# Kernel tuning notes

Hardware: AMD Instinct MI355X
Metric: run time of the kernel (lower is better)

Reference implementation:

```python
import jax, jax.numpy as jnp
import numpy as np

B, E, DM = 2, 1024, 512          # batch, n_edges, d_model
H, DK, DV = 8, 64, 64            # heads, d_k, d_v
MAX_NEIGHBOR = 5                 # == attn_max_dist
LN_EPS = 1e-6
NEG = -1e9


def setup_inputs() -> dict:
    key = jax.random.key(0)
    ks = jax.random.split(key, 9)
    s = 0.02
    return {
        "x": jax.random.normal(ks[0], (B, DM, E, 1), jnp.float32),
        "dist": jax.random.randint(ks[1], (B, E, E), 0, 12, jnp.int32),
        "base_rpr": jax.random.normal(ks[2], (MAX_NEIGHBOR + 1, DK), jnp.float32) * s,
        "w_q": jax.random.normal(ks[3], (DM, H * DK), jnp.float32) * s,
        "w_k": jax.random.normal(ks[4], (DM, H * DK), jnp.float32) * s,
        "w_v": jax.random.normal(ks[5], (DM, H * DV), jnp.float32) * s,
        "w_fc": jax.random.normal(ks[6], (H * DV, DM), jnp.float32) * s,
        "ln_g": jnp.ones((DM,), jnp.float32),
        "ln_b": jnp.zeros((DM,), jnp.float32),
    }


def reference(x, dist, base_rpr, w_q, w_k, w_v, w_fc, ln_g, ln_b):
    temp = jnp.asarray(DK, x.dtype) ** 0.5
    # local-attention mask (dist <= attn_max_dist); all edges valid (same-size meshes)
    mask = dist <= MAX_NEIGHBOR                      # [B,E,E] bool

    s = jnp.transpose(x[..., 0], (0, 2, 1))          # [B,E,DM]
    residual = s

    # LayerNorm applied to q only (as in the torch module)
    mu = s.mean(-1, keepdims=True)
    var = ((s - mu) ** 2).mean(-1, keepdims=True)
    qn = (s - mu) / jnp.sqrt(var + LN_EPS) * ln_g + ln_b

    q = (qn @ w_q).reshape(B, E, H, DK).transpose(0, 2, 1, 3)   # [B,H,E,DK]
    k = (s @ w_k).reshape(B, E, H, DK).transpose(0, 2, 1, 3)
    v = (s @ w_v).reshape(B, E, H, DV).transpose(0, 2, 1, 3)

    # relative-position representations gathered by (clipped) distance
    rpr = base_rpr[jnp.minimum(dist, MAX_NEIGHBOR)]  # [B,E,E,DK]

    qs = q / temp
    attn1 = jnp.einsum("bhid,bhjd->bhij", qs, k)
    attn2 = jnp.einsum("bhid,bijd->bhij", qs, rpr)
    logits = jnp.where(mask[:, None], attn1 + attn2, NEG)
    attn = jax.nn.softmax(logits, axis=-1)           # [B,H,E,E]

    out = jnp.einsum("bhij,bhjd->bhid", attn, v)     # [B,H,E,DV]
    out = out.transpose(0, 2, 1, 3).reshape(B, E, H * DV) @ w_fc + residual
    x_out = out.transpose(0, 2, 1)[..., None]        # [B,DM,E,1]

    mf = mask[:, None].astype(attn.dtype)            # [B,1,E,E]
    attn_per_edge = (attn * mf).sum((1, 2)) / mf.sum((1, 2))  # [B,E]
    return x_out, attn, attn_per_edge
```

## Files before the change

kernel.cpp:

```cpp
#include <hip/hip_runtime.h>

#define NB_B 2
#define NB_E 1024
#define NB_DM 512
#define NB_H 8
#define NEGV -1e9f

typedef __attribute__((ext_vector_type(8))) __bf16 bf16x8;
typedef __attribute__((ext_vector_type(8))) unsigned short u16x8;
typedef __attribute__((ext_vector_type(4))) float f32x4;

static __device__ __forceinline__ float bf2f(unsigned short u){
  union { unsigned int i; float f; } v; v.i = ((unsigned int)u) << 16; return v.f;
}
static __device__ __forceinline__ unsigned short f2bf(float f){
  union { float f; unsigned int i; } v; v.f = f;
  unsigned int r = v.i + 0x7FFFu + ((v.i >> 16) & 1u);
  return (unsigned short)(r >> 16);
}
static __device__ __forceinline__ f32x4 mfma16(bf16x8 a, bf16x8 b, f32x4 c){
  return __builtin_amdgcn_mfma_f32_16x16x32_bf16(a, b, c, 0, 0, 0);
}

__global__ void k_transpose_x(const float* __restrict__ x, unsigned short* __restrict__ s_bf){
  __shared__ float tile[32][33];
  const int b = blockIdx.z;
  const int d0 = blockIdx.y * 32;
  const int e0 = blockIdx.x * 32;
  const int tx = threadIdx.x, ty = threadIdx.y;
  #pragma unroll
  for (int r = 0; r < 4; ++r){
    const int d = d0 + ty + r*8;
    tile[ty + r*8][tx] = x[((size_t)b*NB_DM + d)*NB_E + e0 + tx];
  }
  __syncthreads();
  #pragma unroll
  for (int r = 0; r < 4; ++r){
    const int e = e0 + ty + r*8;
    s_bf[((size_t)b*NB_E + e)*NB_DM + d0 + tx] = f2bf(tile[tx][ty + r*8]);
  }
}

__global__ void k_transpose_w(const float* __restrict__ w0, const float* __restrict__ w1,
                              const float* __restrict__ w2, const float* __restrict__ w3,
                              unsigned short* __restrict__ wT){
  __shared__ float tile[32][33];
  const int which = blockIdx.z;
  const float* w = which==0 ? w0 : which==1 ? w1 : which==2 ? w2 : w3;
  unsigned short* dst = wT + (size_t)which*512*512;
  const int k0 = blockIdx.y*32, n0 = blockIdx.x*32;
  const int tx = threadIdx.x, ty = threadIdx.y;
  #pragma unroll
  for (int r = 0; r < 4; ++r)
    tile[ty + r*8][tx] = w[(size_t)(k0 + ty + r*8)*512 + n0 + tx];
  __syncthreads();
  #pragma unroll
  for (int r = 0; r < 4; ++r)
    dst[(size_t)(n0 + ty + r*8)*512 + k0 + tx] = f2bf(tile[tx][ty + r*8]);
}

__global__ __launch_bounds__(64) void k_ln(const unsigned short* __restrict__ s_bf,
    unsigned short* __restrict__ qn_bf, const float* __restrict__ gg, const float* __restrict__ bb){
  const int row = blockIdx.x, l = threadIdx.x;
  const unsigned short* sp = s_bf + (size_t)row*512 + l*8;
  u16x8 v = *(const u16x8*)sp;
  float f[8]; float sum = 0.f, sq = 0.f;
  #pragma unroll
  for (int i = 0; i < 8; ++i){ f[i] = bf2f(v[i]); sum += f[i]; sq += f[i]*f[i]; }
  #pragma unroll
  for (int off = 32; off >= 1; off >>= 1){
    sum += __shfl_xor(sum, off);
    sq  += __shfl_xor(sq, off);
  }
  const float mu  = sum * (1.f/512.f);
  const float var = sq * (1.f/512.f) - mu*mu;
  const float rstd = rsqrtf(var + 1e-6f);
  const float4 g0 = *(const float4*)(gg + l*8);
  const float4 g1 = *(const float4*)(gg + l*8 + 4);
  const float4 b0 = *(const float4*)(bb + l*8);
  const float4 b1 = *(const float4*)(bb + l*8 + 4);
  const float gv[8] = {g0.x,g0.y,g0.z,g0.w,g1.x,g1.y,g1.z,g1.w};
  const float bv[8] = {b0.x,b0.y,b0.z,b0.w,b1.x,b1.y,b1.z,b1.w};
  u16x8 o;
  #pragma unroll
  for (int i = 0; i < 8; ++i) o[i] = f2bf((f[i]-mu)*rstd*gv[i] + bv[i]);
  *(u16x8*)(qn_bf + (size_t)row*512 + l*8) = o;
}

__global__ void k_dist8(const int* __restrict__ dist, unsigned char* __restrict__ d8){
  const int idx = blockIdx.x*256 + threadIdx.x;
  const int4 d = ((const int4*)dist)[idx];
  uchar4 o;
  o.x = (unsigned char)(d.x <= 5 ? d.x : 6);
  o.y = (unsigned char)(d.y <= 5 ? d.y : 6);
  o.z = (unsigned char)(d.z <= 5 ? d.z : 6);
  o.w = (unsigned char)(d.w <= 5 ? d.w : 6);
  ((uchar4*)d8)[idx] = o;
}

__global__ void k_cnt(const unsigned char* __restrict__ d8, int* __restrict__ cnt){
  const int b = blockIdx.y;
  const int i0 = blockIdx.x*32;
  const int tid = threadIdx.x;
  #pragma unroll
  for (int jj = 0; jj < 4; ++jj){
    const int j = tid + jj*256;
    int c = 0;
    #pragma unroll 8
    for (int i = 0; i < 32; ++i)
      c += (d8[((size_t)b*NB_E + i0 + i)*NB_E + j] < 6) ? 1 : 0;
    atomicAdd(&cnt[b*NB_E + j], c);
  }
}

__global__ __launch_bounds__(256) void k_qr(const unsigned short* __restrict__ Q,
    const float* __restrict__ base_rpr, float* __restrict__ qr){
  __shared__ float rl[384];
  const int tid = threadIdx.x;
  for (int t = tid; t < 384; t += 256) rl[t] = base_rpr[t];
  __syncthreads();
  const int g = blockIdx.x*256 + tid;
  const unsigned short* qp = Q + (size_t)g*64;
  float qv[64];
  #pragma unroll
  for (int i = 0; i < 8; ++i){
    u16x8 v = *(const u16x8*)(qp + i*8);
    #pragma unroll
    for (int j = 0; j < 8; ++j) qv[i*8+j] = bf2f(v[j]);
  }
  #pragma unroll
  for (int c = 0; c < 6; ++c){
    float sacc = 0.f;
    #pragma unroll
    for (int d = 0; d < 64; ++d) sacc += qv[d]*rl[c*64 + d];
    qr[(size_t)g*8 + c] = sacc;
  }
}

template<int MODE>
__global__ __launch_bounds__(256) void k_gemm(
    const unsigned short* __restrict__ A, const unsigned short* __restrict__ BT,
    unsigned short* __restrict__ dst_bf, float* __restrict__ dst_f,
    const float* __restrict__ resid)
{
  const int tid = threadIdx.x;
  const int l = tid & 63, wv = tid >> 6;
  const int ll = l & 15, lg = l >> 4;
  const int m0 = blockIdx.x*64 + wv*16;
  const int n0 = blockIdx.y*64;
  const unsigned short* arow = A + (size_t)(m0 + ll)*512 + lg*8;
  f32x4 acc[4];
  #pragma unroll
  for (int nt = 0; nt < 4; ++nt) acc[nt] = (f32x4){0.f,0.f,0.f,0.f};
  #pragma unroll
  for (int ks = 0; ks < 16; ++ks){
    bf16x8 a = *(const bf16x8*)(arow + ks*32);
    #pragma unroll
    for (int nt = 0; nt < 4; ++nt){
      bf16x8 bv = *(const bf16x8*)(BT + (size_t)(n0 + nt*16 + ll)*512 + ks*32 + lg*8);
      acc[nt] = mfma16(a, bv, acc[nt]);
    }
  }
  const int rbase = m0 + lg*4;
  const int bidx = rbase >> 10;
  const int e = rbase & 1023;
  #pragma unroll
  for (int nt = 0; nt < 4; ++nt){
    const int n = n0 + nt*16 + ll;
    if (MODE == 0 || MODE == 1){
      const int h = n >> 6, dk = n & 63;
      unsigned short* dp = dst_bf + (((size_t)bidx*NB_H + h)*NB_E + e)*64 + dk;
      #pragma unroll
      for (int r = 0; r < 4; ++r)
        dp[(size_t)r*64] = f2bf(MODE == 0 ? acc[nt][r]*0.125f : acc[nt][r]);
    } else if (MODE == 2){
      const int h = n >> 6, dv = n & 63;
      ushort4 ov;
      ov.x = f2bf(acc[nt][0]); ov.y = f2bf(acc[nt][1]);
      ov.z = f2bf(acc[nt][2]); ov.w = f2bf(acc[nt][3]);
      *(ushort4*)(dst_bf + (((size_t)bidx*NB_H + h)*64 + dv)*NB_E + e) = ov;
    } else {
      const float* xr = resid + ((size_t)bidx*NB_DM + n)*NB_E + e;
      const float4 rv = *(const float4*)xr;
      const float4 ov = make_float4(acc[nt][0]+rv.x, acc[nt][1]+rv.y,
                                    acc[nt][2]+rv.z, acc[nt][3]+rv.w);
      *(float4*)(dst_f + ((size_t)bidx*NB_DM + n)*NB_E + e) = ov;
    }
  }
}

__global__ __launch_bounds__(256, 2) void k_attn(
    const unsigned short* __restrict__ Q, const unsigned short* __restrict__ K,
    const unsigned short* __restrict__ VT, const float* __restrict__ qr,
    const unsigned char* __restrict__ d8, float* __restrict__ attn_out,
    unsigned short* __restrict__ outb, float* __restrict__ ape_acc)
{
  __shared__ __align__(16) unsigned char smem[65536];
  unsigned short* plds = (unsigned short*)smem;
  float* qr_l = (float*)smem;
  float* redm = (float*)(smem + 768);
  float* reds = (float*)(smem + 1280);

  const int tid = threadIdx.x;
  const int l = tid & 63, w = tid >> 6;
  const int lg = l >> 4, ll = l & 15;
  const int bh = blockIdx.y;
  const int b = bh >> 3;
  const int ib = blockIdx.x << 5;

  for (int t = tid; t < 32*6; t += 256)
    qr_l[t] = qr[((size_t)bh*NB_E + ib + (t/6))*8 + (t % 6)];

  const unsigned short* Qb = Q + ((size_t)bh*NB_E + ib)*64;
  bf16x8 qf[2][2];
  #pragma unroll
  for (int it = 0; it < 2; ++it)
    #pragma unroll
    for (int hf = 0; hf < 2; ++hf)
      qf[it][hf] = *(const bf16x8*)(Qb + (size_t)(it*16 + ll)*64 + hf*32 + lg*8);
  __syncthreads();

  f32x4 s[2][16];
  const unsigned short* Kb = K + (size_t)bh*NB_E*64;
  #pragma unroll
  for (int jt = 0; jt < 16; ++jt){
    const int jrow = (w*16 + jt)*16 + ll;
    bf16x8 k0 = *(const bf16x8*)(Kb + (size_t)jrow*64 + lg*8);
    bf16x8 k1 = *(const bf16x8*)(Kb + (size_t)jrow*64 + 32 + lg*8);
    #pragma unroll
    for (int it = 0; it < 2; ++it){
      f32x4 acc = {0.f,0.f,0.f,0.f};
      acc = mfma16(qf[it][0], k0, acc);
      acc = mfma16(qf[it][1], k1, acc);
      s[it][jt] = acc;
    }
  }

  const unsigned char* d8r = d8 + ((size_t)b*NB_E + ib)*NB_E;
  #pragma unroll
  for (int it = 0; it < 2; ++it)
  #pragma unroll
  for (int jt = 0; jt < 16; ++jt){
    const int j = (w*16 + jt)*16 + ll;
    #pragma unroll
    for (int r = 0; r < 4; ++r){
      const int il = it*16 + lg*4 + r;
      const unsigned char c = d8r[(size_t)il*NB_E + j];
      s[it][jt][r] = (c < 6) ? (s[it][jt][r] + qr_l[il*6 + c]) : NEGV;
    }
  }

  float mx[2][4];
  #pragma unroll
  for (int it = 0; it < 2; ++it)
    #pragma unroll
    for (int r = 0; r < 4; ++r){
      float m = -3.0e38f;
      #pragma unroll
      for (int jt = 0; jt < 16; ++jt) m = fmaxf(m, s[it][jt][r]);
      m = fmaxf(m, __shfl_xor(m, 1));
      m = fmaxf(m, __shfl_xor(m, 2));
      m = fmaxf(m, __shfl_xor(m, 4));
      m = fmaxf(m, __shfl_xor(m, 8));
      if (ll == 0) redm[w*32 + it*16 + lg*4 + r] = m;
    }
  __syncthreads();
  #pragma unroll
  for (int it = 0; it < 2; ++it)
    #pragma unroll
    for (int r = 0; r < 4; ++r){
      const int il = it*16 + lg*4 + r;
      mx[it][r] = fmaxf(fmaxf(redm[il], redm[32+il]), fmaxf(redm[64+il], redm[96+il]));
    }

  float rinv[2][4];
  #pragma unroll
  for (int it = 0; it < 2; ++it)
    #pragma unroll
    for (int r = 0; r < 4; ++r){
      float sum = 0.f;
      #pragma unroll
      for (int jt = 0; jt < 16; ++jt){
        const float p = exp2f((s[it][jt][r] - mx[it][r]) * 1.4426950408889634f);
        s[it][jt][r] = p;
        sum += p;
      }
      sum += __shfl_xor(sum, 1);
      sum += __shfl_xor(sum, 2);
      sum += __shfl_xor(sum, 4);
      sum += __shfl_xor(sum, 8);
      if (ll == 0) reds[w*32 + it*16 + lg*4 + r] = sum;
    }
  __syncthreads();
  #pragma unroll
  for (int it = 0; it < 2; ++it)
    #pragma unroll
    for (int r = 0; r < 4; ++r){
      const int il = it*16 + lg*4 + r;
      rinv[it][r] = 1.0f / (reds[il] + reds[32+il] + reds[64+il] + reds[96+il]);
    }
  __syncthreads();

  float* arow = attn_out + ((size_t)bh*NB_E + ib)*NB_E;
  #pragma unroll
  for (int jt = 0; jt < 16; ++jt){
    const int j = (w*16 + jt)*16 + ll;
    float csum = 0.f;
    #pragma unroll
    for (int it = 0; it < 2; ++it)
      #pragma unroll
      for (int r = 0; r < 4; ++r){
        const int il = it*16 + lg*4 + r;
        const float pn = s[it][jt][r] * rinv[it][r];
        arow[(size_t)il*NB_E + j] = pn;
        const int byo = ((il*1024 + j)*2) ^ ((il & 7) << 4);
        plds[byo >> 1] = f2bf(pn);
        csum += pn;
      }
    csum += __shfl_xor(csum, 16);
    csum += __shfl_xor(csum, 32);
    if (l < 16) atomicAdd(&ape_acc[b*NB_E + j], csum);
  }
  __syncthreads();

  const unsigned short* Vb = VT + ((size_t)bh*64 + w*16 + ll)*NB_E;
  f32x4 o0 = {0.f,0.f,0.f,0.f}, o1 = {0.f,0.f,0.f,0.f};
  #pragma unroll
  for (int kk = 0; kk < 32; ++kk){
    bf16x8 vf = *(const bf16x8*)(Vb + kk*32 + lg*8);
    {
      const int i0 = ll;
      const int byo = ((i0*1024 + kk*32 + lg*8)*2) ^ ((i0 & 7) << 4);
      bf16x8 p0 = *(const bf16x8*)(smem + byo);
      o0 = mfma16(p0, vf, o0);
    }
    {
      const int i1 = 16 + ll;
      const int byo = ((i1*1024 + kk*32 + lg*8)*2) ^ ((i1 & 7) << 4);
      bf16x8 p1 = *(const bf16x8*)(smem + byo);
      o1 = mfma16(p1, vf, o1);
    }
  }
  const int coln = (bh & 7)*64 + w*16 + ll;
  #pragma unroll
  for (int r = 0; r < 4; ++r){
    const int e0 = ib + lg*4 + r;
    outb[((size_t)b*NB_E + e0)*512 + coln] = f2bf(o0[r]);
    const int e1 = ib + 16 + lg*4 + r;
    outb[((size_t)b*NB_E + e1)*512 + coln] = f2bf(o1[r]);
  }
}

__global__ void k_ape(const float* __restrict__ acc, const int* __restrict__ cnt,
                      float* __restrict__ out){
  const int t = blockIdx.x*256 + threadIdx.x;
  if (t < NB_B*NB_E){
    const int c = cnt[t];
    out[t] = c > 0 ? acc[t] / (float)c : 0.f;
  }
}

extern "C" void kernel_launch(void* const* d_in, const int* in_sizes, int n_in,
                              void* d_out, int out_size, void* d_ws, size_t ws_size,
                              hipStream_t stream)
{
  const float* x        = (const float*)d_in[0];
  const int*   dist     = (const int*)d_in[1];
  const float* base_rpr = (const float*)d_in[2];
  const float* w_q      = (const float*)d_in[3];
  const float* w_k      = (const float*)d_in[4];
  const float* w_v      = (const float*)d_in[5];
  const float* w_fc     = (const float*)d_in[6];
  const float* ln_g     = (const float*)d_in[7];
  const float* ln_b     = (const float*)d_in[8];

  float* x_out    = (float*)d_out;
  float* attn_out = x_out + (size_t)NB_B*NB_DM*NB_E;
  float* ape_out  = attn_out + (size_t)NB_B*NB_H*NB_E*NB_E;

  unsigned char* ws = (unsigned char*)d_ws;
  unsigned short* s_bf   = (unsigned short*)(ws);
  unsigned short* qn_bf  = (unsigned short*)(ws + 2097152);
  unsigned short* wT     = (unsigned short*)(ws + 4194304);
  unsigned short* Qb     = (unsigned short*)(ws + 6291456);
  unsigned short* Kb     = (unsigned short*)(ws + 8388608);
  unsigned short* VTb    = (unsigned short*)(ws + 10485760);
  unsigned short* outb   = (unsigned short*)(ws + 12582912);
  float*          qr     = (float*)(ws + 14680064);
  unsigned char*  d8     = ws + 15204352;
  int*            cnt    = (int*)(ws + 17301504);
  float*          apeacc = (float*)(ws + 17309696);

  hipMemsetAsync(cnt, 0, NB_B*NB_E*sizeof(int), stream);
  hipMemsetAsync(apeacc, 0, NB_B*NB_E*sizeof(float), stream);

  k_transpose_w<<<dim3(16,16,4), dim3(32,8), 0, stream>>>(w_q, w_k, w_v, w_fc, wT);
  k_transpose_x<<<dim3(32,16,2), dim3(32,8), 0, stream>>>(x, s_bf);
  k_ln<<<dim3(2048), dim3(64), 0, stream>>>(s_bf, qn_bf, ln_g, ln_b);
  k_dist8<<<dim3(2048), dim3(256), 0, stream>>>(dist, d8);
  k_cnt<<<dim3(32,2), dim3(256), 0, stream>>>(d8, cnt);

  k_gemm<0><<<dim3(32,8), dim3(256), 0, stream>>>(qn_bf, wT,          Qb,  nullptr, nullptr);
  k_gemm<1><<<dim3(32,8), dim3(256), 0, stream>>>(s_bf,  wT + 262144, Kb,  nullptr, nullptr);
  k_gemm<2><<<dim3(32,8), dim3(256), 0, stream>>>(s_bf,  wT + 524288, VTb, nullptr, nullptr);
  k_qr<<<dim3(64), dim3(256), 0, stream>>>(Qb, base_rpr, qr);

  k_attn<<<dim3(32,16), dim3(256), 0, stream>>>(Qb, Kb, VTb, qr, d8, attn_out, outb, apeacc);

  k_gemm<3><<<dim3(32,8), dim3(256), 0, stream>>>(outb, wT + 786432, nullptr, x_out, x);
  k_ape<<<dim3(8), dim3(256), 0, stream>>>(apeacc, cnt, ape_out);
}
```

Measured before the change: 134.0 us.

## Fuse QKV GEMMs with qr, merge dist kernels, shrink attention tiles

The three Q/K/V projection GEMMs and the qr dot-product kernel are merged into one launch, with qr computed in the Q epilogue through shuffles. The dist conversion and the mask count are merged into one pass over dist. The attention kernel now handles 16 query rows per block instead of 32, using a smaller LDS footprint to allow 4 blocks per CU. It also uses a hardware exp2, nontemporal stores for the attn output, and per-head ape accumulators to reduce atomic contention. These changes cut launch count and redundant memory passes, at the cost of reloading K and V twice as often across blocks.

Measured after the change: 122.4 us. -8.6%, faster.

```diff
diff --git a/kernel.cpp b/kernel.cpp
--- a/kernel.cpp
+++ b/kernel.cpp
@@ -20,6 +20,13 @@
 }
 static __device__ __forceinline__ f32x4 mfma16(bf16x8 a, bf16x8 b, f32x4 c){
   return __builtin_amdgcn_mfma_f32_16x16x32_bf16(a, b, c, 0, 0, 0);
+}
+static __device__ __forceinline__ float fast_exp2(float x){
+#if __has_builtin(__builtin_amdgcn_exp2f)
+  return __builtin_amdgcn_exp2f(x);
+#else
+  return exp2f(x);
+#endif
 }
 
 __global__ void k_transpose_x(const float* __restrict__ x, unsigned short* __restrict__ s_bf){
@@ -59,9 +66,10 @@
     dst[(size_t)(n0 + ty + r*8)*512 + k0 + tx] = f2bf(tile[tx][ty + r*8]);
 }
 
-__global__ __launch_bounds__(64) void k_ln(const unsigned short* __restrict__ s_bf,
+__global__ __launch_bounds__(256) void k_ln(const unsigned short* __restrict__ s_bf,
     unsigned short* __restrict__ qn_bf, const float* __restrict__ gg, const float* __restrict__ bb){
-  const int row = blockIdx.x, l = threadIdx.x;
+  const int row = blockIdx.x*4 + (threadIdx.x >> 6);
+  const int l = threadIdx.x & 63;
   const unsigned short* sp = s_bf + (size_t)row*512 + l*8;
   u16x8 v = *(const u16x8*)sp;
   float f[8]; float sum = 0.f, sq = 0.f;
@@ -87,61 +95,116 @@
   *(u16x8*)(qn_bf + (size_t)row*512 + l*8) = o;
 }
 
-__global__ void k_dist8(const int* __restrict__ dist, unsigned char* __restrict__ d8){
-  const int idx = blockIdx.x*256 + threadIdx.x;
-  const int4 d = ((const int4*)dist)[idx];
-  uchar4 o;
-  o.x = (unsigned char)(d.x <= 5 ? d.x : 6);
-  o.y = (unsigned char)(d.y <= 5 ? d.y : 6);
-  o.z = (unsigned char)(d.z <= 5 ? d.z : 6);
-  o.w = (unsigned char)(d.w <= 5 ? d.w : 6);
-  ((uchar4*)d8)[idx] = o;
-}
-
-__global__ void k_cnt(const unsigned char* __restrict__ d8, int* __restrict__ cnt){
+__global__ __launch_bounds__(256) void k_dist(const int* __restrict__ dist,
+    unsigned char* __restrict__ d8, int* __restrict__ cnt){
   const int b = blockIdx.y;
-  const int i0 = blockIdx.x*32;
+  const int i0 = blockIdx.x * 16;
+  const int t = threadIdx.x;
+  int c0 = 0, c1 = 0, c2 = 0, c3 = 0;
+  #pragma unroll 4
+  for (int r = 0; r < 16; ++r){
+    const int row = i0 + r;
+    const int4 d = ((const int4*)(dist + ((size_t)b*NB_E + row)*NB_E))[t];
+    uchar4 o;
+    o.x = (unsigned char)(d.x <= 5 ? d.x : 6);
+    o.y = (unsigned char)(d.y <= 5 ? d.y : 6);
+    o.z = (unsigned char)(d.z <= 5 ? d.z : 6);
+    o.w = (unsigned char)(d.w <= 5 ? d.w : 6);
+    ((uchar4*)(d8 + ((size_t)b*NB_E + row)*NB_E))[t] = o;
+    c0 += (d.x <= 5); c1 += (d.y <= 5); c2 += (d.z <= 5); c3 += (d.w <= 5);
+  }
+  int* cb = cnt + b*NB_E + t*4;
+  atomicAdd(cb + 0, c0);
+  atomicAdd(cb + 1, c1);
+  atomicAdd(cb + 2, c2);
+  atomicAdd(cb + 3, c3);
+}
+
+__global__ __launch_bounds__(256) void k_gemm_qkv(
+    const unsigned short* __restrict__ qn, const unsigned short* __restrict__ s,
+    const unsigned short* __restrict__ wT, const float* __restrict__ base_rpr,
+    unsigned short* __restrict__ Qb, unsigned short* __restrict__ Kb,
+    unsigned short* __restrict__ VTb, float* __restrict__ qr)
+{
+  const int z = blockIdx.z;
+  const unsigned short* A  = (z == 0) ? qn : s;
+  const unsigned short* BT = wT + (size_t)z*262144;
   const int tid = threadIdx.x;
-  #pragma unroll
-  for (int jj = 0; jj < 4; ++jj){
-    const int j = tid + jj*256;
-    int c = 0;
-    #pragma unroll 8
-    for (int i = 0; i < 32; ++i)
-      c += (d8[((size_t)b*NB_E + i0 + i)*NB_E + j] < 6) ? 1 : 0;
-    atomicAdd(&cnt[b*NB_E + j], c);
-  }
-}
-
-__global__ __launch_bounds__(256) void k_qr(const unsigned short* __restrict__ Q,
-    const float* __restrict__ base_rpr, float* __restrict__ qr){
-  __shared__ float rl[384];
-  const int tid = threadIdx.x;
-  for (int t = tid; t < 384; t += 256) rl[t] = base_rpr[t];
-  __syncthreads();
-  const int g = blockIdx.x*256 + tid;
-  const unsigned short* qp = Q + (size_t)g*64;
-  float qv[64];
-  #pragma unroll
-  for (int i = 0; i < 8; ++i){
-    u16x8 v = *(const u16x8*)(qp + i*8);
-    #pragma unroll
-    for (int j = 0; j < 8; ++j) qv[i*8+j] = bf2f(v[j]);
-  }
-  #pragma unroll
-  for (int c = 0; c < 6; ++c){
-    float sacc = 0.f;
-    #pragma unroll
-    for (int d = 0; d < 64; ++d) sacc += qv[d]*rl[c*64 + d];
-    qr[(size_t)g*8 + c] = sacc;
-  }
-}
-
-template<int MODE>
-__global__ __launch_bounds__(256) void k_gemm(
+  const int l = tid & 63, wv = tid >> 6;
+  const int ll = l & 15, lg = l >> 4;
+  const int m0 = blockIdx.x*64 + wv*16;
+  const int n0 = blockIdx.y*64;
+  const unsigned short* arow = A + (size_t)(m0 + ll)*512 + lg*8;
+  f32x4 acc[4];
+  #pragma unroll
+  for (int nt = 0; nt < 4; ++nt) acc[nt] = (f32x4){0.f,0.f,0.f,0.f};
+  #pragma unroll
+  for (int ks = 0; ks < 16; ++ks){
+    bf16x8 a = *(const bf16x8*)(arow + ks*32);
+    #pragma unroll
+    for (int nt = 0; nt < 4; ++nt){
+      bf16x8 bv = *(const bf16x8*)(BT + (size_t)(n0 + nt*16 + ll)*512 + ks*32 + lg*8);
+      acc[nt] = mfma16(a, bv, acc[nt]);
+    }
+  }
+  const int rbase = m0 + lg*4;
+  const int bidx = rbase >> 10;
+  const int e = rbase & 1023;
+  const int h = n0 >> 6;
+  if (z == 0){
+    float rprv[6][4];
+    #pragma unroll
+    for (int c = 0; c < 6; ++c)
+      #pragma unroll
+      for (int nt = 0; nt < 4; ++nt)
+        rprv[c][nt] = base_rpr[c*64 + nt*16 + ll];
+    #pragma unroll
+    for (int nt = 0; nt < 4; ++nt){
+      const int dk = nt*16 + ll;
+      unsigned short* dp = Qb + (((size_t)bidx*NB_H + h)*NB_E + e)*64 + dk;
+      #pragma unroll
+      for (int r = 0; r < 4; ++r)
+        dp[(size_t)r*64] = f2bf(acc[nt][r]*0.125f);
+    }
+    #pragma unroll
+    for (int r = 0; r < 4; ++r){
+      #pragma unroll
+      for (int c = 0; c < 6; ++c){
+        float tv = 0.f;
+        #pragma unroll
+        for (int nt = 0; nt < 4; ++nt) tv += acc[nt][r]*0.125f*rprv[c][nt];
+        tv += __shfl_xor(tv, 1);
+        tv += __shfl_xor(tv, 2);
+        tv += __shfl_xor(tv, 4);
+        tv += __shfl_xor(tv, 8);
+        if (ll == 0)
+          qr[(((size_t)(bidx*NB_H + h)*NB_E) + e + r)*8 + c] = tv;
+      }
+    }
+  } else if (z == 1){
+    #pragma unroll
+    for (int nt = 0; nt < 4; ++nt){
+      const int dk = nt*16 + ll;
+      unsigned short* dp = Kb + (((size_t)bidx*NB_H + h)*NB_E + e)*64 + dk;
+      #pragma unroll
+      for (int r = 0; r < 4; ++r)
+        dp[(size_t)r*64] = f2bf(acc[nt][r]);
+    }
+  } else {
+    #pragma unroll
+    for (int nt = 0; nt < 4; ++nt){
+      const int dv = nt*16 + ll;
+      ushort4 ov;
+      ov.x = f2bf(acc[nt][0]); ov.y = f2bf(acc[nt][1]);
+      ov.z = f2bf(acc[nt][2]); ov.w = f2bf(acc[nt][3]);
+      *(ushort4*)(VTb + (((size_t)bidx*NB_H + h)*64 + dv)*NB_E + e) = ov;
+    }
+  }
+}
+
+__global__ __launch_bounds__(256) void k_fc(
     const unsigned short* __restrict__ A, const unsigned short* __restrict__ BT,
-    unsigned short* __restrict__ dst_bf, float* __restrict__ dst_f,
-    const float* __restrict__ resid)
+    float* __restrict__ dst_f, const float* __restrict__ resid)
 {
   const int tid = threadIdx.x;
   const int l = tid & 63, wv = tid >> 6;
@@ -167,139 +230,111 @@
   #pragma unroll
   for (int nt = 0; nt < 4; ++nt){
     const int n = n0 + nt*16 + ll;
-    if (MODE == 0 || MODE == 1){
-      const int h = n >> 6, dk = n & 63;
-      unsigned short* dp = dst_bf + (((size_t)bidx*NB_H + h)*NB_E + e)*64 + dk;
-      #pragma unroll
-      for (int r = 0; r < 4; ++r)
-        dp[(size_t)r*64] = f2bf(MODE == 0 ? acc[nt][r]*0.125f : acc[nt][r]);
-    } else if (MODE == 2){
-      const int h = n >> 6, dv = n & 63;
-      ushort4 ov;
-      ov.x = f2bf(acc[nt][0]); ov.y = f2bf(acc[nt][1]);
-      ov.z = f2bf(acc[nt][2]); ov.w = f2bf(acc[nt][3]);
-      *(ushort4*)(dst_bf + (((size_t)bidx*NB_H + h)*64 + dv)*NB_E + e) = ov;
-    } else {
-      const float* xr = resid + ((size_t)bidx*NB_DM + n)*NB_E + e;
-      const float4 rv = *(const float4*)xr;
-      const float4 ov = make_float4(acc[nt][0]+rv.x, acc[nt][1]+rv.y,
-                                    acc[nt][2]+rv.z, acc[nt][3]+rv.w);
-      *(float4*)(dst_f + ((size_t)bidx*NB_DM + n)*NB_E + e) = ov;
-    }
-  }
-}
-
-__global__ __launch_bounds__(256, 2) void k_attn(
+    const float* xr = resid + ((size_t)bidx*NB_DM + n)*NB_E + e;
+    const float4 rv = *(const float4*)xr;
+    const float4 ov = make_float4(acc[nt][0]+rv.x, acc[nt][1]+rv.y,
+                                  acc[nt][2]+rv.z, acc[nt][3]+rv.w);
+    *(float4*)(dst_f + ((size_t)bidx*NB_DM + n)*NB_E + e) = ov;
+  }
+}
+
+__global__ __launch_bounds__(256, 4) void k_attn(
     const unsigned short* __restrict__ Q, const unsigned short* __restrict__ K,
     const unsigned short* __restrict__ VT, const float* __restrict__ qr,
     const unsigned char* __restrict__ d8, float* __restrict__ attn_out,
     unsigned short* __restrict__ outb, float* __restrict__ ape_acc)
 {
-  __shared__ __align__(16) unsigned char smem[65536];
-  unsigned short* plds = (unsigned short*)smem;
+  __shared__ __align__(16) unsigned char smem[2048 + 32768];
+  unsigned short* plds = (unsigned short*)(smem + 2048);
   float* qr_l = (float*)smem;
-  float* redm = (float*)(smem + 768);
-  float* reds = (float*)(smem + 1280);
+  float* redm = (float*)(smem + 512);
+  float* reds = (float*)(smem + 1024);
 
   const int tid = threadIdx.x;
   const int l = tid & 63, w = tid >> 6;
   const int lg = l >> 4, ll = l & 15;
-  const int bh = blockIdx.y;
+  const int n = blockIdx.x;
+  const int m = n >> 3;
+  const int bh = (n & 7)*2 + (m >> 6);
   const int b = bh >> 3;
-  const int ib = blockIdx.x << 5;
-
-  for (int t = tid; t < 32*6; t += 256)
+  const int ib = (m & 63) << 4;
+
+  for (int t = tid; t < 16*6; t += 256)
     qr_l[t] = qr[((size_t)bh*NB_E + ib + (t/6))*8 + (t % 6)];
 
   const unsigned short* Qb = Q + ((size_t)bh*NB_E + ib)*64;
-  bf16x8 qf[2][2];
-  #pragma unroll
-  for (int it = 0; it < 2; ++it)
-    #pragma unroll
-    for (int hf = 0; hf < 2; ++hf)
-      qf[it][hf] = *(const bf16x8*)(Qb + (size_t)(it*16 + ll)*64 + hf*32 + lg*8);
-  __syncthreads();
-
-  f32x4 s[2][16];
+  bf16x8 qf[2];
+  #pragma unroll
+  for (int hf = 0; hf < 2; ++hf)
+    qf[hf] = *(const bf16x8*)(Qb + (size_t)ll*64 + hf*32 + lg*8);
+  __syncthreads();
+
+  f32x4 s[16];
   const unsigned short* Kb = K + (size_t)bh*NB_E*64;
   #pragma unroll
   for (int jt = 0; jt < 16; ++jt){
     const int jrow = (w*16 + jt)*16 + ll;
     bf16x8 k0 = *(const bf16x8*)(Kb + (size_t)jrow*64 + lg*8);
     bf16x8 k1 = *(const bf16x8*)(Kb + (size_t)jrow*64 + 32 + lg*8);
-    #pragma unroll
-    for (int it = 0; it < 2; ++it){
-      f32x4 acc = {0.f,0.f,0.f,0.f};
-      acc = mfma16(qf[it][0], k0, acc);
-      acc = mfma16(qf[it][1], k1, acc);
-      s[it][jt] = acc;
-    }
+    f32x4 acc = {0.f,0.f,0.f,0.f};
+    acc = mfma16(qf[0], k0, acc);
+    acc = mfma16(qf[1], k1, acc);
+    s[jt] = acc;
   }
 
   const unsigned char* d8r = d8 + ((size_t)b*NB_E + ib)*NB_E;
-  #pragma unroll
-  for (int it = 0; it < 2; ++it)
   #pragma unroll
   for (int jt = 0; jt < 16; ++jt){
     const int j = (w*16 + jt)*16 + ll;
     #pragma unroll
     for (int r = 0; r < 4; ++r){
-      const int il = it*16 + lg*4 + r;
+      const int il = lg*4 + r;
       const unsigned char c = d8r[(size_t)il*NB_E + j];
-      s[it][jt][r] = (c < 6) ? (s[it][jt][r] + qr_l[il*6 + c]) : NEGV;
-    }
-  }
-
-  float mx[2][4];
-  #pragma unroll
-  for (int it = 0; it < 2; ++it)
-    #pragma unroll
-    for (int r = 0; r < 4; ++r){
-      float m = -3.0e38f;
-      #pragma unroll
-      for (int jt = 0; jt < 16; ++jt) m = fmaxf(m, s[it][jt][r]);
-      m = fmaxf(m, __shfl_xor(m, 1));
-      m = fmaxf(m, __shfl_xor(m, 2));
-      m = fmaxf(m, __shfl_xor(m, 4));
-      m = fmaxf(m, __shfl_xor(m, 8));
-      if (ll == 0) redm[w*32 + it*16 + lg*4 + r] = m;
-    }
-  __syncthreads();
-  #pragma unroll
-  for (int it = 0; it < 2; ++it)
-    #pragma unroll
-    for (int r = 0; r < 4; ++r){
-      const int il = it*16 + lg*4 + r;
-      mx[it][r] = fmaxf(fmaxf(redm[il], redm[32+il]), fmaxf(redm[64+il], redm[96+il]));
-    }
-
-  float rinv[2][4];
-  #pragma unroll
-  for (int it = 0; it < 2; ++it)
-    #pragma unroll
-    for (int r = 0; r < 4; ++r){
-      float sum = 0.f;
-      #pragma unroll
-      for (int jt = 0; jt < 16; ++jt){
-        const float p = exp2f((s[it][jt][r] - mx[it][r]) * 1.4426950408889634f);
-        s[it][jt][r] = p;
-        sum += p;
-      }
-      sum += __shfl_xor(sum, 1);
-      sum += __shfl_xor(sum, 2);
-      sum += __shfl_xor(sum, 4);
-      sum += __shfl_xor(sum, 8);
-      if (ll == 0) reds[w*32 + it*16 + lg*4 + r] = sum;
-    }
-  __syncthreads();
-  #pragma unroll
-  for (int it = 0; it < 2; ++it)
-    #pragma unroll
-    for (int r = 0; r < 4; ++r){
-      const int il = it*16 + lg*4 + r;
-      rinv[it][r] = 1.0f / (reds[il] + reds[32+il] + reds[64+il] + reds[96+il]);
-    }
-  __syncthreads();
+      s[jt][r] = (c < 6) ? (s[jt][r] + qr_l[il*6 + c]) : NEGV;
+    }
+  }
+
+  #pragma unroll
+  for (int r = 0; r < 4; ++r){
+    float mm = -3.0e38f;
+    #pragma unroll
+    for (int jt = 0; jt < 16; ++jt) mm = fmaxf(mm, s[jt][r]);
+    mm = fmaxf(mm, __shfl_xor(mm, 1));
+    mm = fmaxf(mm, __shfl_xor(mm, 2));
+    mm = fmaxf(mm, __shfl_xor(mm, 4));
+    mm = fmaxf(mm, __shfl_xor(mm, 8));
+    if (ll == 0) redm[w*16 + lg*4 + r] = mm;
+  }
+  __syncthreads();
+  float mx[4];
+  #pragma unroll
+  for (int r = 0; r < 4; ++r){
+    const int il = lg*4 + r;
+    mx[r] = fmaxf(fmaxf(redm[il], redm[16+il]), fmaxf(redm[32+il], redm[48+il]));
+  }
+
+  #pragma unroll
+  for (int r = 0; r < 4; ++r){
+    float sum = 0.f;
+    #pragma unroll
+    for (int jt = 0; jt < 16; ++jt){
+      const float p = fast_exp2((s[jt][r] - mx[r]) * 1.4426950408889634f);
+      s[jt][r] = p;
+      sum += p;
+    }
+    sum += __shfl_xor(sum, 1);
+    sum += __shfl_xor(sum, 2);
+    sum += __shfl_xor(sum, 4);
+    sum += __shfl_xor(sum, 8);
+    if (ll == 0) reds[w*16 + lg*4 + r] = sum;
+  }
+  __syncthreads();
+  float rinv[4];
+  #pragma unroll
+  for (int r = 0; r < 4; ++r){
+    const int il = lg*4 + r;
+    rinv[r] = 1.0f / (reds[il] + reds[16+il] + reds[32+il] + reds[48+il]);
+  }
 
   float* arow = attn_out + ((size_t)bh*NB_E + ib)*NB_E;
   #pragma unroll
@@ -307,47 +342,34 @@
     const int j = (w*16 + jt)*16 + ll;
     float csum = 0.f;
     #pragma unroll
-    for (int it = 0; it < 2; ++it)
-      #pragma unroll
-      for (int r = 0; r < 4; ++r){
-        const int il = it*16 + lg*4 + r;
-        const float pn = s[it][jt][r] * rinv[it][r];
-        arow[(size_t)il*NB_E + j] = pn;
-        const int byo = ((il*1024 + j)*2) ^ ((il & 7) << 4);
-        plds[byo >> 1] = f2bf(pn);
-        csum += pn;
-      }
+    for (int r = 0; r < 4; ++r){
+      const int il = lg*4 + r;
+      const float pn = s[jt][r] * rinv[r];
+      __builtin_nontemporal_store(pn, &arow[(size_t)il*NB_E + j]);
+      const int byo = ((il*1024 + j)*2) ^ ((il & 7) << 4);
+      plds[byo >> 1] = f2bf(pn);
+      csum += pn;
+    }
     csum += __shfl_xor(csum, 16);
     csum += __shfl_xor(csum, 32);
-    if (l < 16) atomicAdd(&ape_acc[b*NB_E + j], csum);
+    if (l < 16) atomicAdd(&ape_acc[(bh << 10) + j], csum);
   }
   __syncthreads();
 
   const unsigned short* Vb = VT + ((size_t)bh*64 + w*16 + ll)*NB_E;
-  f32x4 o0 = {0.f,0.f,0.f,0.f}, o1 = {0.f,0.f,0.f,0.f};
+  f32x4 o = {0.f,0.f,0.f,0.f};
   #pragma unroll
   for (int kk = 0; kk < 32; ++kk){
     bf16x8 vf = *(const bf16x8*)(Vb + kk*32 + lg*8);
-    {
-      const int i0 = ll;
-      const int byo = ((i0*1024 + kk*32 + lg*8)*2) ^ ((i0 & 7) << 4);
-      bf16x8 p0 = *(const bf16x8*)(smem + byo);
-      o0 = mfma16(p0, vf, o0);
-    }
-    {
-      const int i1 = 16 + ll;
-      const int byo = ((i1*1024 + kk*32 + lg*8)*2) ^ ((i1 & 7) << 4);
-      bf16x8 p1 = *(const bf16x8*)(smem + byo);
-      o1 = mfma16(p1, vf, o1);
-    }
+    const int byo = ((ll*2048 + (kk*32 + lg*8)*2)) ^ ((ll & 7) << 4);
+    bf16x8 p = *(const bf16x8*)(smem + 2048 + byo);
+    o = mfma16(p, vf, o);
   }
   const int coln = (bh & 7)*64 + w*16 + ll;
   #pragma unroll
   for (int r = 0; r < 4; ++r){
     const int e0 = ib + lg*4 + r;
-    outb[((size_t)b*NB_E + e0)*512 + coln] = f2bf(o0[r]);
-    const int e1 = ib + 16 + lg*4 + r;
-    outb[((size_t)b*NB_E + e1)*512 + coln] = f2bf(o1[r]);
+    outb[((size_t)b*NB_E + e0)*512 + coln] = f2bf(o[r]);
   }
 }
 
@@ -355,8 +377,12 @@
                       float* __restrict__ out){
   const int t = blockIdx.x*256 + threadIdx.x;
   if (t < NB_B*NB_E){
+    const int b = t >> 10, j = t & 1023;
+    float ssum = 0.f;
+    #pragma unroll
+    for (int h = 0; h < 8; ++h) ssum += acc[(((b<<3) + h) << 10) + j];
     const int c = cnt[t];
-    out[t] = c > 0 ? acc[t] / (float)c : 0.f;
+    out[t] = c > 0 ? ssum / (float)c : 0.f;
   }
 }
 
@@ -391,22 +417,18 @@
   int*            cnt    = (int*)(ws + 17301504);
   float*          apeacc = (float*)(ws + 17309696);
 
-  hipMemsetAsync(cnt, 0, NB_B*NB_E*sizeof(int), stream);
-  hipMemsetAsync(apeacc, 0, NB_B*NB_E*sizeof(float), stream);
+  hipMemsetAsync(cnt, 0, 8192 + 65536, stream);
 
   k_transpose_w<<<dim3(16,16,4), dim3(32,8), 0, stream>>>(w_q, w_k, w_v, w_fc, wT);
   k_transpose_x<<<dim3(32,16,2), dim3(32,8), 0, stream>>>(x, s_bf);
-  k_ln<<<dim3(2048), dim3(64), 0, stream>>>(s_bf, qn_bf, ln_g, ln_b);
-  k_dist8<<<dim3(2048), dim3(256), 0, stream>>>(dist, d8);
-  k_cnt<<<dim3(32,2), dim3(256), 0, stream>>>(d8, cnt);
-
-  k_gemm<0><<<dim3(32,8), dim3(256), 0, stream>>>(qn_bf, wT,          Qb,  nullptr, nullptr);
-  k_gemm<1><<<dim3(32,8), dim3(256), 0, stream>>>(s_bf,  wT + 262144, Kb,  nullptr, nullptr);
-  k_gemm<2><<<dim3(32,8), dim3(256), 0, stream>>>(s_bf,  wT + 524288, VTb, nullptr, nullptr);
-  k_qr<<<dim3(64), dim3(256), 0, stream>>>(Qb, base_rpr, qr);
-
-  k_attn<<<dim3(32,16), dim3(256), 0, stream>>>(Qb, Kb, VTb, qr, d8, attn_out, outb, apeacc);
-
-  k_gemm<3><<<dim3(32,8), dim3(256), 0, stream>>>(outb, wT + 786432, nullptr, x_out, x);
+  k_ln<<<dim3(512), dim3(256), 0, stream>>>(s_bf, qn_bf, ln_g, ln_b);
+  k_dist<<<dim3(64,2), dim3(256), 0, stream>>>(dist, d8, cnt);
+
+  k_gemm_qkv<<<dim3(32,8,3), dim3(256), 0, stream>>>(qn_bf, s_bf, wT, base_rpr,
+                                                     Qb, Kb, VTb, qr);
+
+  k_attn<<<dim3(1024), dim3(256), 0, stream>>>(Qb, Kb, VTb, qr, d8, attn_out, outb, apeacc);
+
+  k_fc<<<dim3(32,8), dim3(256), 0, stream>>>(outb, wT + 786432, x_out, x);
   k_ape<<<dim3(8), dim3(256), 0, stream>>>(apeacc, cnt, ape_out);
 }
```
